# Kernel optimization log

Hardware: AMD Instinct MI355X
Metric: run time of the kernel (lower is better)

The kernel has to match this reference:

```python
import jax, jax.numpy as jnp
import numpy as np

N = 100000      # nodes
E = 1600000     # graph edges
P = 800000      # hypergraph incidence pairs
HE = 20000      # hyperedges
F_IN = 128      # node features
DIM = 64        # hidden dim (hard-coded in module)
NC = 40         # num_classes


def _lin_init(key, fan_in, fan_out):
    k1, k2 = jax.random.split(key)
    s = 1.0 / np.sqrt(fan_in)
    W = jax.random.uniform(k1, (fan_in, fan_out), jnp.float32, -s, s)
    b = jax.random.uniform(k2, (fan_out,), jnp.float32, -s, s)
    return W, b


def setup_inputs() -> dict:
    key = jax.random.key(0)
    ks = jax.random.split(key, 10)
    x = jax.random.normal(ks[0], (N, F_IN), jnp.float32)
    edge_index = jax.random.randint(ks[1], (2, E), 0, N, dtype=jnp.int64)
    node_idx = jax.random.randint(ks[2], (P,), 0, N, dtype=jnp.int64)
    he_idx = jax.random.randint(ks[3], (P,), 0, HE, dtype=jnp.int64)
    hyperedge_index = jnp.stack([node_idx, he_idx], axis=0)
    W_h1, b_h1 = _lin_init(ks[4], F_IN, DIM)
    W_h2, b_h2 = _lin_init(ks[5], DIM, DIM)
    W_c1, b_c1 = _lin_init(ks[6], F_IN + DIM, DIM)
    W_c2, b_c2 = _lin_init(ks[7], DIM, NC)
    W_lp, b_lp = _lin_init(ks[8], NC, NC)
    return dict(x=x, edge_index=edge_index, hyperedge_index=hyperedge_index,
                W_h1=W_h1, b_h1=b_h1, W_h2=W_h2, b_h2=b_h2,
                W_c1=W_c1, b_c1=b_c1, W_c2=W_c2, b_c2=b_c2,
                W_lp=W_lp, b_lp=b_lp)


def hypergraph_conv(x, node_idx, he_idx, W, b):
    # PyG HypergraphConv (no attention, hyperedge_weight = 1):
    # out = D^{-1} H B^{-1} H^T (x W) + b
    xw = x @ W                                    # [N, D]
    ones = jnp.ones(node_idx.shape[0], xw.dtype)
    Dn = jax.ops.segment_sum(ones, node_idx, num_segments=N)   # node degree
    Bh = jax.ops.segment_sum(ones, he_idx, num_segments=HE)    # hyperedge size
    D_inv = jnp.where(Dn > 0, 1.0 / Dn, 0.0)
    B_inv = jnp.where(Bh > 0, 1.0 / Bh, 0.0)
    # node -> hyperedge: m_e = (1/|e|) sum_{i in e} xw[i]
    msg1 = xw[node_idx] * B_inv[he_idx][:, None]               # [P, D]
    e_feat = jax.ops.segment_sum(msg1, he_idx, num_segments=HE)
    # hyperedge -> node: out_i = (1/deg(i)) sum_{e ni i} m_e
    msg2 = e_feat[he_idx] * D_inv[node_idx][:, None]           # [P, D]
    out = jax.ops.segment_sum(msg2, node_idx, num_segments=N)
    return out + b


def gcn_conv(x, edge_index, W, b):
    # PyG GCNConv: add self-loops, symmetric normalization
    xw = x @ W                                    # [N, D]
    loop = jnp.arange(N, dtype=edge_index.dtype)
    src = jnp.concatenate([edge_index[0], loop])
    dst = jnp.concatenate([edge_index[1], loop])
    deg = jax.ops.segment_sum(jnp.ones(dst.shape[0], xw.dtype), dst, num_segments=N)
    dis = jnp.where(deg > 0, jax.lax.rsqrt(deg), 0.0)
    norm = dis[src] * dis[dst]                    # [E+N]
    out = jax.ops.segment_sum(xw[src] * norm[:, None], dst, num_segments=N)
    return out + b


def reference(x, edge_index, hyperedge_index,
              W_h1, b_h1, W_h2, b_h2, W_c1, b_c1, W_c2, b_c2, W_lp, b_lp):
    node_idx, he_idx = hyperedge_index[0], hyperedge_index[1]
    x_hyper = jax.nn.relu(hypergraph_conv(x, node_idx, he_idx, W_h1, b_h1))
    # dropout is identity in eval mode
    x_hyper = hypergraph_conv(x_hyper, node_idx, he_idx, W_h2, b_h2)
    xc = jnp.concatenate([x, x_hyper], axis=1)    # [N, F_IN + DIM]
    x_gnn = jax.nn.relu(gcn_conv(xc, edge_index, W_c1, b_c1))
    x_gnn = gcn_conv(x_gnn, edge_index, W_c2, b_c2)
    return x_gnn @ W_lp + b_lp                     # [N, NC]
```

## Files before the change

### kernel.cpp

```cpp
#include <hip/hip_runtime.h>
#include <hip/hip_bf16.h>


typedef __attribute__((ext_vector_type(8))) short s16x8;
typedef __attribute__((ext_vector_type(4))) float f32x4;

__device__ __forceinline__ float ldf(const void* p, int f32, long long i) {
    if (f32) return ((const float*)p)[i];
    unsigned v = ((unsigned)((const unsigned short*)p)[i]) << 16;
    return __uint_as_float(v);
}

__device__ __forceinline__ int ldi(const int* __restrict__ w, int i64, long long i, int lim) {
    int v = i64 ? w[2 * i] : w[i];
    return ((unsigned)v < (unsigned)lim) ? v : 0;
}

__device__ __forceinline__ float b2f(unsigned short u) {
    return __uint_as_float(((unsigned)u) << 16);
}
__device__ __forceinline__ unsigned short f2b(float f) {
    __hip_bfloat16 h = __float2bfloat16(f);
    return *reinterpret_cast<unsigned short*>(&h);
}
__device__ __forceinline__ float4 b2f4(ushort4 u) {
    return make_float4(b2f(u.x), b2f(u.y), b2f(u.z), b2f(u.w));
}
__device__ __forceinline__ ushort4 f2b4(float4 v) {
    ushort4 u; u.x = f2b(v.x); u.y = f2b(v.y); u.z = f2b(v.z); u.w = f2b(v.w);
    return u;
}

struct DPtrs { const void* p[13]; int n[13]; };

__global__ void detect_k(DPtrs dp, int* __restrict__ flags) {
    int b = blockIdx.x;
    __shared__ int cnt;
    if (threadIdx.x == 0) cnt = 0;
    __syncthreads();
    int c = 0;
    if (b < 11) {
        const unsigned short* u = (const unsigned short*)dp.p[b];
        int np = dp.n[b]; if (np > 2048) np = 2048;
        for (int i = threadIdx.x; i < np; i += blockDim.x) {
            unsigned e = (u[i] >> 7) & 0xFFu;
            if (e != 0u && (e < 90u || e > 160u)) c++;
        }
        atomicAdd(&cnt, c);
        __syncthreads();
        if (threadIdx.x == 0) flags[b] = (cnt * 8 > np) ? 1 : 0;
    } else {
        const int* w = (const int*)dp.p[b];
        int np = dp.n[b]; if (np > 1024) np = 1024;
        for (int i = threadIdx.x; i < np; i += blockDim.x)
            if (w[2 * i + 1] != 0) c++;
        atomicAdd(&cnt, c);
        __syncthreads();
        if (threadIdx.x == 0) flags[b] = (cnt == 0) ? 1 : 0;
    }
}

struct Item { int b1; unsigned p1; int b2; unsigned p2; };

__device__ __forceinline__ Item decode(const int* __restrict__ ew, const int* __restrict__ hw,
                                       const int* __restrict__ FL, long long i,
                                       int E, int P, int N, int HE, int shN, int shH) {
    Item it; it.b2 = -1; it.p2 = 0;
    if (i < E) {
        int g = FL[11];
        int key = ldi(ew, g, (long long)E + i, N);
        int val = ldi(ew, g, i, N);
        it.b1 = key >> shN;
        it.p1 = ((unsigned)(key & ((1 << shN) - 1)) << 20) | (unsigned)val;
    } else {
        long long j = i - E;
        int g = FL[12];
        int nd = ldi(hw, g, j, N);
        int he = ldi(hw, g, (long long)P + j, HE);
        it.b1 = 256 + (nd >> shN);
        it.p1 = ((unsigned)(nd & ((1 << shN) - 1)) << 20) | (unsigned)he;
        it.b2 = 512 + (he >> shH);
        it.p2 = ((unsigned)(he & ((1 << shH) - 1)) << 20) | (unsigned)nd;
    }
    return it;
}

__global__ void bucket_count_k(const int* __restrict__ ew, const int* __restrict__ hw,
                               const int* __restrict__ FL, int* __restrict__ gcnt,
                               int E, int P, int N, int HE, int shN, int shH) {
    __shared__ int hist[768];
    int t = threadIdx.x;
    for (int b = t; b < 768; b += 256) hist[b] = 0;
    __syncthreads();
    long long T = (long long)E + P;
    long long stride = (long long)gridDim.x * 256;
    for (long long i = (long long)blockIdx.x * 256 + t; i < T; i += stride) {
        Item it = decode(ew, hw, FL, i, E, P, N, HE, shN, shH);
        atomicAdd(&hist[it.b1], 1);
        if (it.b2 >= 0) atomicAdd(&hist[it.b2], 1);
    }
    __syncthreads();
    for (int b = t; b < 768; b += 256) {
        int h = hist[b];
        if (h) atomicAdd(&gcnt[b], h);
    }
}

__global__ void bucket_scan_k(const int* __restrict__ gcnt, int* __restrict__ bkOff,
                              int* __restrict__ gcur, int E, int P) {
    __shared__ int sh[256];
    int t = threadIdx.x;
    long long rbase[3] = {0, (long long)E, (long long)E + P};
    for (int c = 0; c < 3; c++) {
        int v = gcnt[c * 256 + t];
        sh[t] = v;
        __syncthreads();
        for (int o = 1; o < 256; o <<= 1) {
            int y = (t >= o) ? sh[t - o] : 0;
            __syncthreads();
            sh[t] += y;
            __syncthreads();
        }
        int excl = sh[t] - v;
        bkOff[c * 256 + t] = excl;
        gcur[c * 256 + t] = (int)(rbase[c] + excl);
        __syncthreads();
    }
}

#define PCHUNK 8192

__global__ void bucket_place_k(const int* __restrict__ ew, const int* __restrict__ hw,
                               const int* __restrict__ FL, int* __restrict__ gcur,
                               unsigned* __restrict__ pbuf,
                               int E, int P, int N, int HE, int shN, int shH) {
    __shared__ int hist[768];
    __shared__ int cur[768];
    long long T = (long long)E + P;
    long long start = (long long)blockIdx.x * PCHUNK;
    long long end = start + PCHUNK; if (end > T) end = T;
    int t = threadIdx.x;
    for (int b = t; b < 768; b += 256) hist[b] = 0;
    __syncthreads();
    for (long long i = start + t; i < end; i += 256) {
        Item it = decode(ew, hw, FL, i, E, P, N, HE, shN, shH);
        atomicAdd(&hist[it.b1], 1);
        if (it.b2 >= 0) atomicAdd(&hist[it.b2], 1);
    }
    __syncthreads();
    for (int b = t; b < 768; b += 256) {
        int h = hist[b];
        cur[b] = h ? atomicAdd(&gcur[b], h) : 0;
    }
    __syncthreads();
    for (long long i = start + t; i < end; i += 256) {
        Item it = decode(ew, hw, FL, i, E, P, N, HE, shN, shH);
        int s1 = atomicAdd(&cur[it.b1], 1);
        pbuf[s1] = it.p1;
        if (it.b2 >= 0) {
            int s2 = atomicAdd(&cur[it.b2], 1);
            pbuf[s2] = it.p2;
        }
    }
}

__global__ void build_k(const unsigned* __restrict__ pbuf,
                        const int* __restrict__ gcnt, const int* __restrict__ bkOff,
                        int* __restrict__ eoff, int* __restrict__ ecnt, int* __restrict__ esrc,
                        int* __restrict__ poffN, int* __restrict__ pcntN, int* __restrict__ pheL,
                        int* __restrict__ poffH, int* __restrict__ pcntH, int* __restrict__ pniL,
                        int E, int P, int N, int HE, int shN, int shH) {
    __shared__ int hist[512];
    __shared__ int offs[512];
    __shared__ int s2[256];
    int b = blockIdx.x, t = threadIdx.x;
    int csr = b >> 8, lb = b & 255;
    int sh    = (csr == 2) ? shH : shN;
    int nkeys = (csr == 2) ? HE : N;
    int span = 1 << sh;
    int keyBase = lb << sh;
    if (keyBase >= nkeys) return;
    int keyEnd = keyBase + span; if (keyEnd > nkeys) keyEnd = nkeys;
    int cnt = gcnt[b];
    long long rbase = (csr == 0) ? 0 : ((csr == 1) ? (long long)E : (long long)E + P);
    long long pstart = rbase + bkOff[b];
    int lstBase = bkOff[b];
    int* off  = (csr == 0) ? eoff : ((csr == 1) ? poffN : poffH);
    int* cntA = (csr == 0) ? ecnt : ((csr == 1) ? pcntN : pcntH);
    int* lst  = (csr == 0) ? esrc : ((csr == 1) ? pheL : pniL);

    for (int k = t; k < 512; k += 256) hist[k] = 0;
    __syncthreads();
    for (int i = t; i < cnt; i += 256)
        atomicAdd(&hist[pbuf[pstart + i] >> 20], 1);
    __syncthreads();
    int a0 = hist[2 * t], a1 = hist[2 * t + 1];
    s2[t] = a0 + a1;
    __syncthreads();
    for (int o = 1; o < 256; o <<= 1) {
        int y = (t >= o) ? s2[t - o] : 0;
        __syncthreads();
        s2[t] += y;
        __syncthreads();
    }
    int excl = s2[t] - (a0 + a1);
    offs[2 * t] = excl;
    offs[2 * t + 1] = excl + a0;
    __syncthreads();
    for (int k = keyBase + t; k < keyEnd; k += 256) {
        off[k]  = lstBase + offs[k - keyBase];
        cntA[k] = hist[k - keyBase];
    }
    __syncthreads();
    for (int i = t; i < cnt; i += 256) {
        unsigned u = pbuf[pstart + i];
        int lk = u >> 20;
        int slot = atomicAdd(&offs[lk], 1);
        lst[lstBase + slot] = (int)(u & 0xFFFFFu);
    }
}

__global__ void norms_k(const int* __restrict__ ecnt, const int* __restrict__ pcntN,
                        const int* __restrict__ pcntH, float* __restrict__ dis,
                        float* __restrict__ Dinv, float* __restrict__ Binv, int N, int HE) {
    int i = blockIdx.x * blockDim.x + threadIdx.x;
    if (i < N) dis[i] = rsqrtf((float)(ecnt[i] + 1));
    else if (i < 2 * N) { int c = pcntN[i - N]; Dinv[i - N] = c ? (1.f / (float)c) : 0.f; }
    else if (i < 2 * N + HE) { int c = pcntH[i - 2 * N]; Binv[i - 2 * N] = c ? (1.f / (float)c) : 0.f; }
}

__global__ void wlp2_k(const void* Wc2, const int* fWc2, const void* Wlp, const int* fWlp,
                       const void* bc2, const int* fbc2, const void* blp, const int* fblp,
                       float* __restrict__ Wlp2, float* __restrict__ bias2, int NC) {
    extern __shared__ float sm[];
    float* sW2 = sm;
    float* sLP = sm + 64 * NC;
    int t = threadIdx.x;
    int fw2 = fWc2[0], flp = fWlp[0];
    for (int e = t; e < 64 * NC; e += blockDim.x) sW2[e] = ldf(Wc2, fw2, e);
    for (int e = t; e < NC * NC; e += blockDim.x) sLP[e] = ldf(Wlp, flp, e);
    __syncthreads();
    for (int e = t; e < 64 * NC; e += blockDim.x) {
        int r = e / NC, c = e % NC;
        float s = 0.f;
        for (int k = 0; k < NC; k++) s = fmaf(sW2[r * NC + k], sLP[k * NC + c], s);
        Wlp2[e] = s;
    }
    if (t < NC) {
        float s = ldf(blp, fblp[0], t);
        int fb2 = fbc2[0];
        for (int k = 0; k < NC; k++) s = fmaf(ldf(bc2, fb2, k), sLP[k * NC + t], s);
        bias2[t] = s;
    }
}

__global__ void gat_n2e_k(const ushort4* __restrict__ xw, const int* __restrict__ off,
                          const int* __restrict__ cnt, const int* __restrict__ lst,
                          const float* __restrict__ Binv, ushort4* __restrict__ ef, int HE) {
    int idx = blockIdx.x * blockDim.x + threadIdx.x;
    int e = idx >> 4, l = idx & 15;
    if (e >= HE) return;
    int o = off[e], c = cnt[e];
    float4 a = make_float4(0.f, 0.f, 0.f, 0.f);
    int j = 0;
    for (; j + 4 <= c; j += 4) {
        int s0 = lst[o + j], s1 = lst[o + j + 1], s2 = lst[o + j + 2], s3 = lst[o + j + 3];
        float4 v0 = b2f4(xw[((long long)s0 << 4) + l]);
        float4 v1 = b2f4(xw[((long long)s1 << 4) + l]);
        float4 v2 = b2f4(xw[((long long)s2 << 4) + l]);
        float4 v3 = b2f4(xw[((long long)s3 << 4) + l]);
        a.x += (v0.x + v1.x) + (v2.x + v3.x);
        a.y += (v0.y + v1.y) + (v2.y + v3.y);
        a.z += (v0.z + v1.z) + (v2.z + v3.z);
        a.w += (v0.w + v1.w) + (v2.w + v3.w);
    }
    for (; j < c; j++) {
        float4 v = b2f4(xw[((long long)lst[o + j] << 4) + l]);
        a.x += v.x; a.y += v.y; a.z += v.z; a.w += v.w;
    }
    float bi = Binv[e];
    a.x *= bi; a.y *= bi; a.z *= bi; a.w *= bi;
    ef[((long long)e << 4) + l] = f2b4(a);
}

template <bool RELU>
__global__ void gat_e2n_k(const ushort4* __restrict__ ef, const int* __restrict__ off,
                          const int* __restrict__ cnt, const int* __restrict__ lst,
                          const float* __restrict__ Dinv, const void* __restrict__ bias,
                          const int* __restrict__ fb, ushort4* __restrict__ out, int N) {
    int idx = blockIdx.x * blockDim.x + threadIdx.x;
    int w = idx >> 4, l = idx & 15;
    if (w >= N) return;
    int o = off[w], c = cnt[w];
    float4 a = make_float4(0.f, 0.f, 0.f, 0.f);
    int j = 0;
    for (; j + 4 <= c; j += 4) {
        int s0 = lst[o + j], s1 = lst[o + j + 1], s2 = lst[o + j + 2], s3 = lst[o + j + 3];
        float4 v0 = b2f4(ef[((long long)s0 << 4) + l]);
        float4 v1 = b2f4(ef[((long long)s1 << 4) + l]);
        float4 v2 = b2f4(ef[((long long)s2 << 4) + l]);
        float4 v3 = b2f4(ef[((long long)s3 << 4) + l]);
        a.x += (v0.x + v1.x) + (v2.x + v3.x);
        a.y += (v0.y + v1.y) + (v2.y + v3.y);
        a.z += (v0.z + v1.z) + (v2.z + v3.z);
        a.w += (v0.w + v1.w) + (v2.w + v3.w);
    }
    for (; j < c; j++) {
        float4 v = b2f4(ef[((long long)lst[o + j] << 4) + l]);
        a.x += v.x; a.y += v.y; a.z += v.z; a.w += v.w;
    }
    float di = Dinv[w];
    int fbv = fb[0];
    float4 b = make_float4(ldf(bias, fbv, 4 * l), ldf(bias, fbv, 4 * l + 1),
                           ldf(bias, fbv, 4 * l + 2), ldf(bias, fbv, 4 * l + 3));
    a.x = a.x * di + b.x; a.y = a.y * di + b.y;
    a.z = a.z * di + b.z; a.w = a.w * di + b.w;
    if (RELU) {
        a.x = fmaxf(a.x, 0.f); a.y = fmaxf(a.y, 0.f);
        a.z = fmaxf(a.z, 0.f); a.w = fmaxf(a.w, 0.f);
    }
    out[((long long)w << 4) + l] = f2b4(a);
}

template <bool RELU>
__global__ void gcn_gat_k(const ushort4* __restrict__ y, const int* __restrict__ off,
                          const int* __restrict__ cnt, const int* __restrict__ lst,
                          const float* __restrict__ dis, const void* __restrict__ bias,
                          const int* __restrict__ fb, ushort4* __restrict__ out, int N) {
    int idx = blockIdx.x * blockDim.x + threadIdx.x;
    int w = idx >> 4, l = idx & 15;
    if (w >= N) return;
    int o = off[w], c = cnt[w];
    float4 a = b2f4(y[((long long)w << 4) + l]);
    int j = 0;
    for (; j + 4 <= c; j += 4) {
        int s0 = lst[o + j], s1 = lst[o + j + 1], s2 = lst[o + j + 2], s3 = lst[o + j + 3];
        float4 v0 = b2f4(y[((long long)s0 << 4) + l]);
        float4 v1 = b2f4(y[((long long)s1 << 4) + l]);
        float4 v2 = b2f4(y[((long long)s2 << 4) + l]);
        float4 v3 = b2f4(y[((long long)s3 << 4) + l]);
        a.x += (v0.x + v1.x) + (v2.x + v3.x);
        a.y += (v0.y + v1.y) + (v2.y + v3.y);
        a.z += (v0.z + v1.z) + (v2.z + v3.z);
        a.w += (v0.w + v1.w) + (v2.w + v3.w);
    }
    for (; j < c; j++) {
        float4 v = b2f4(y[((long long)lst[o + j] << 4) + l]);
        a.x += v.x; a.y += v.y; a.z += v.z; a.w += v.w;
    }
    float dd = dis[w];
    int fbv = fb[0];
    float4 b = make_float4(ldf(bias, fbv, 4 * l), ldf(bias, fbv, 4 * l + 1),
                           ldf(bias, fbv, 4 * l + 2), ldf(bias, fbv, 4 * l + 3));
    a.x = a.x * dd + b.x; a.y = a.y * dd + b.y;
    a.z = a.z * dd + b.z; a.w = a.w * dd + b.w;
    if (RELU) {
        a.x = fmaxf(a.x, 0.f); a.y = fmaxf(a.y, 0.f);
        a.z = fmaxf(a.z, 0.f); a.w = fmaxf(a.w, 0.f);
    }
    out[((long long)w << 4) + l] = f2b4(a);
}

__global__ void gcn_gatM_k(const ushort4* __restrict__ y2, const int* __restrict__ off,
                           const int* __restrict__ cnt, const int* __restrict__ lst,
                           const float* __restrict__ dis, const float* __restrict__ bias2,
                           float4* __restrict__ out4, int N, int nc4, int npw) {
    int idx = blockIdx.x * blockDim.x + threadIdx.x;
    int wave = idx >> 6, l64 = idx & 63;
    int grp = l64 / 10, li = l64 - grp * 10;
    if (nc4 != 10) { grp = l64 / nc4; li = l64 - grp * nc4; }
    int w = wave * npw + grp;
    if (grp >= npw || w >= N) return;
    int o = off[w], c = cnt[w];
    float4 a = b2f4(y2[(long long)w * nc4 + li]);
    int j = 0;
    for (; j + 4 <= c; j += 4) {
        int s0 = lst[o + j], s1 = lst[o + j + 1], s2 = lst[o + j + 2], s3 = lst[o + j + 3];
        float4 v0 = b2f4(y2[(long long)s0 * nc4 + li]);
        float4 v1 = b2f4(y2[(long long)s1 * nc4 + li]);
        float4 v2 = b2f4(y2[(long long)s2 * nc4 + li]);
        float4 v3 = b2f4(y2[(long long)s3 * nc4 + li]);
        a.x += (v0.x + v1.x) + (v2.x + v3.x);
        a.y += (v0.y + v1.y) + (v2.y + v3.y);
        a.z += (v0.z + v1.z) + (v2.z + v3.z);
        a.w += (v0.w + v1.w) + (v2.w + v3.w);
    }
    for (; j < c; j++) {
        float4 v = b2f4(y2[(long long)lst[o + j] * nc4 + li]);
        a.x += v.x; a.y += v.y; a.z += v.z; a.w += v.w;
    }
    float dd = dis[w];
    float4 b = *(const float4*)&bias2[4 * li];
    a.x = a.x * dd + b.x; a.y = a.y * dd + b.y;
    a.z = a.z * dd + b.z; a.w = a.w * dd + b.w;
    out4[(long long)w * nc4 + li] = a;
}

__device__ __forceinline__ s16x8 load8bf(const void* A, int af, long long base) {
    s16x8 o;
    if (af) {
        float4 v0 = *(const float4*)((const float*)A + base);
        float4 v1 = *(const float4*)((const float*)A + base + 4);
        o[0] = (short)f2b(v0.x); o[1] = (short)f2b(v0.y);
        o[2] = (short)f2b(v0.z); o[3] = (short)f2b(v0.w);
        o[4] = (short)f2b(v1.x); o[5] = (short)f2b(v1.y);
        o[6] = (short)f2b(v1.z); o[7] = (short)f2b(v1.w);
    } else {
        o = *(const s16x8*)&((const unsigned short*)A)[base];
    }
    return o;
}

template <int KK, int MM, bool CATMODE, bool ABF16, bool SCALE>
__global__ __launch_bounds__(256)
void gemm_mfma_k(const void* __restrict__ A, const int* __restrict__ fA,
                 const unsigned short* __restrict__ A2,
                 const void* __restrict__ B, const int* __restrict__ fB,
                 const float* __restrict__ dscale,
                 unsigned short* __restrict__ C, int NR) {
    constexpr int BM = 128;
    constexpr int Kp = KK + 8;
    constexpr int MT = (MM + 15) / 16;
    constexpr int CPR = KK / 8;
    static_assert(KK % 32 == 0, "K must be multiple of 32");

    __shared__ __align__(16) unsigned short As[BM * Kp];
    __shared__ __align__(16) unsigned short Bs[MT * 16 * Kp];

    const int t = threadIdx.x;
    const long long m0 = (long long)blockIdx.x * BM;
    const int af = fA ? fA[0] : 1;
    const int bfv = fB ? fB[0] : 1;

    for (int idx = t; idx < BM * CPR; idx += 256) {
        int r = idx / CPR;
        int kc = (idx - r * CPR) * 8;
        long long gr = m0 + r;
        s16x8 v = {0, 0, 0, 0, 0, 0, 0, 0};
        if (gr < NR) {
            if constexpr (CATMODE) {
                if (kc < 128) v = load8bf(A, af, gr * 128 + kc);
                else v = *(const s16x8*)&A2[gr * 64 + (kc - 128)];
            } else if constexpr (ABF16) {
                v = *(const s16x8*)&((const unsigned short*)A)[gr * KK + kc];
            } else {
                v = load8bf(A, af, gr * (long long)KK + kc);
            }
        }
        *(s16x8*)&As[r * Kp + kc] = v;
    }

    for (int e = t; e < KK * MM; e += 256) {
        int k = e / MM;
        int n = e - k * MM;
        Bs[n * Kp + k] = f2b(ldf(B, bfv, e));
    }
    if constexpr (MT * 16 != MM) {
        for (int e = t; e < (MT * 16 - MM) * KK; e += 256) {
            int n = MM + e / KK;
            int k = e - (e / KK) * KK;
            Bs[n * Kp + k] = 0;
        }
    }
    __syncthreads();

    const int wid = t >> 6, lane = t & 63;
    const int r0 = wid * 32;
    const int arow = lane & 15;
    const int kgrp = lane >> 4;

    f32x4 acc0[MT] = {};
    f32x4 acc1[MT] = {};
#pragma unroll
    for (int kc = 0; kc < KK; kc += 32) {
        const int kb = kc + kgrp * 8;
        s16x8 a0 = *(const s16x8*)&As[(r0 + arow) * Kp + kb];
        s16x8 a1 = *(const s16x8*)&As[(r0 + 16 + arow) * Kp + kb];
#pragma unroll
        for (int m = 0; m < MT; m++) {
            s16x8 b = *(const s16x8*)&Bs[(m * 16 + arow) * Kp + kb];
            acc0[m] = __builtin_amdgcn_mfma_f32_16x16x32_bf16(a0, b, acc0[m], 0, 0, 0);
            acc1[m] = __builtin_amdgcn_mfma_f32_16x16x32_bf16(a1, b, acc1[m], 0, 0, 0);
        }
    }

    const int col0 = lane & 15;
    const int rsub = (lane >> 4) * 4;
#pragma unroll
    for (int h = 0; h < 2; h++) {
#pragma unroll
        for (int i = 0; i < 4; i++) {
            long long r = m0 + r0 + h * 16 + rsub + i;
            if (r < NR) {
                float s = SCALE ? dscale[r] : 1.f;
#pragma unroll
                for (int m = 0; m < MT; m++) {
                    int col = m * 16 + col0;
                    float val = h ? acc1[m][i] : acc0[m][i];
                    if (MT * 16 == MM || col < MM)
                        C[r * MM + col] = f2b(val * s);
                }
            }
        }
    }
}

static inline dim3 g1d(long long n, int b) { return dim3((unsigned)((n + b - 1) / b)); }
static inline int imin(int a, int b) { return a < b ? a : b; }

extern "C" void kernel_launch(void* const* d_in, const int* in_sizes, int n_in,
                              void* d_out, int out_size, void* d_ws, size_t ws_size,
                              hipStream_t stream) {
    const int N  = in_sizes[0] / 128;
    const int E  = in_sizes[1] / 2;
    const int P  = in_sizes[2] / 2;
    const int HE = 20000;
    const int NC = in_sizes[9] / 64;
    const int nc4 = NC / 4;
    const int npw = 64 / nc4;

    const void* x    = d_in[0];
    const int*  ew   = (const int*)d_in[1];
    const int*  hw   = (const int*)d_in[2];
    const void* W_h1 = d_in[3];
    const void* b_h1 = d_in[4];
    const void* W_h2 = d_in[5];
    const void* b_h2 = d_in[6];
    const void* W_c1 = d_in[7];
    const void* b_c1 = d_in[8];
    const void* W_c2 = d_in[9];
    const void* b_c2 = d_in[10];
    const void* W_lp = d_in[11];
    const void* b_lp = d_in[12];

    int shN = 0; while (((N - 1) >> shN) >= 256) shN++;
    int shH = 0; while (((HE - 1) >> shH) >= 256) shH++;

    char* wp = (char*)d_ws;
    auto allocF = [&](size_t n) { float* p = (float*)wp; wp += n * 4; return p; };
    auto allocI = [&](size_t n) { int* p = (int*)wp; wp += n * 4; return p; };
    unsigned short* ub  = (unsigned short*)allocF((size_t)N * 32);
    unsigned short* hb  = (unsigned short*)allocF((size_t)N * 32);
    unsigned short* efb = (unsigned short*)allocF((size_t)HE * 32);
    float* dis   = allocF(N);
    float* Dinv  = allocF(N);
    float* Binv  = allocF(HE);
    float* Wlp2  = allocF((size_t)64 * NC);
    float* bias2 = allocF(NC);
    int* ecnt  = allocI(N);
    int* pcntN = allocI(N);
    int* pcntH = allocI(HE);
    int* eoff  = allocI(N);
    int* poffN = allocI(N);
    int* poffH = allocI(HE);
    int* esrc  = allocI(E);
    int* pheL  = allocI(P);
    int* pniL  = allocI(P);
    int* gBkt  = allocI(768);
    int* bkOff = allocI(768);
    int* gcur  = allocI(768);
    int* FL    = allocI(16);
    unsigned* pbuf = (unsigned*)allocI((size_t)E + 2 * (size_t)P);

    dim3 b256(256), d1(1);

    DPtrs dp;
    const void* farr[11] = {x, W_h1, b_h1, W_h2, b_h2, W_c1, b_c1, W_c2, b_c2, W_lp, b_lp};
    const int   fsz[11]  = {in_sizes[0], in_sizes[3], in_sizes[4], in_sizes[5], in_sizes[6],
                            in_sizes[7], in_sizes[8], in_sizes[9], in_sizes[10], in_sizes[11],
                            in_sizes[12]};
    for (int i = 0; i < 11; ++i) { dp.p[i] = farr[i]; dp.n[i] = fsz[i]; }
    dp.p[11] = ew; dp.n[11] = imin(E, 1024);
    dp.p[12] = hw; dp.n[12] = imin(P, 1024);
    detect_k<<<dim3(13), b256, 0, stream>>>(dp, FL);
    const int* fX   = FL + 0;
    const int* fWh1 = FL + 1,  *fbh1 = FL + 2;
    const int* fWh2 = FL + 3,  *fbh2 = FL + 4;
    const int* fWc1 = FL + 5,  *fbc1 = FL + 6;
    const int* fWc2 = FL + 7,  *fbc2 = FL + 8;
    const int* fWlp = FL + 9,  *fblp = FL + 10;

    hipMemsetAsync(gBkt, 0, 768 * 4, stream);
    bucket_count_k<<<dim3(512), b256, 0, stream>>>(ew, hw, FL, gBkt, E, P, N, HE, shN, shH);
    bucket_scan_k<<<d1, b256, 0, stream>>>(gBkt, bkOff, gcur, E, P);
    {
        long long T = (long long)E + P;
        int nChunks = (int)((T + PCHUNK - 1) / PCHUNK);
        bucket_place_k<<<dim3(nChunks), b256, 0, stream>>>(ew, hw, FL, gcur, pbuf,
                                                           E, P, N, HE, shN, shH);
    }
    build_k<<<dim3(768), b256, 0, stream>>>(pbuf, gBkt, bkOff,
                                            eoff, ecnt, esrc,
                                            poffN, pcntN, pheL,
                                            poffH, pcntH, pniL,
                                            E, P, N, HE, shN, shH);

    norms_k<<<g1d(2 * N + HE, 256), b256, 0, stream>>>(ecnt, pcntN, pcntH, dis, Dinv, Binv, N, HE);
    wlp2_k<<<d1, b256, (64 * NC + NC * NC) * 4, stream>>>(
        W_c2, fWc2, W_lp, fWlp, b_c2, fbc2, b_lp, fblp, Wlp2, bias2, NC);

    const dim3 mfmaGrid((N + 127) / 128);
    const dim3 gatN16(g1d((long long)N * 16, 256));
    const dim3 gatH16(g1d((long long)HE * 16, 256));
    const dim3 gatNC(g1d((long long)((N + npw - 1) / npw) * 64, 256));

    gemm_mfma_k<128, 64, false, false, false><<<mfmaGrid, b256, 0, stream>>>(
        x, fX, nullptr, W_h1, fWh1, nullptr, ub, N);
    gat_n2e_k<<<gatH16, b256, 0, stream>>>((const ushort4*)ub, poffH, pcntH, pniL, Binv, (ushort4*)efb, HE);
    gat_e2n_k<true><<<gatN16, b256, 0, stream>>>((const ushort4*)efb, poffN, pcntN, pheL, Dinv, b_h1, fbh1, (ushort4*)hb, N);

    gemm_mfma_k<64, 64, false, true, false><<<mfmaGrid, b256, 0, stream>>>(
        hb, nullptr, nullptr, W_h2, fWh2, nullptr, ub, N);
    gat_n2e_k<<<gatH16, b256, 0, stream>>>((const ushort4*)ub, poffH, pcntH, pniL, Binv, (ushort4*)efb, HE);
    gat_e2n_k<false><<<gatN16, b256, 0, stream>>>((const ushort4*)efb, poffN, pcntN, pheL, Dinv, b_h2, fbh2, (ushort4*)hb, N);

    gemm_mfma_k<192, 64, true, false, true><<<mfmaGrid, b256, 0, stream>>>(
        x, fX, hb, W_c1, fWc1, dis, ub, N);
    gcn_gat_k<true><<<gatN16, b256, 0, stream>>>((const ushort4*)ub, eoff, ecnt, esrc, dis, b_c1, fbc1, (ushort4*)hb, N);

    gemm_mfma_k<64, 40, false, true, true><<<mfmaGrid, b256, 0, stream>>>(
        hb, nullptr, nullptr, Wlp2, nullptr, dis, ub, N);
    gcn_gatM_k<<<gatNC, b256, 0, stream>>>((const ushort4*)ub, eoff, ecnt, esrc, dis, bias2, (float4*)d_out, N, nc4, npw);
}
```

Baseline: 485.4 us.

## Pretranspose weights once and load GEMM operands directly from global memory

Adds a small kernel that converts and transposes all four weight matrices to padded bf16 once, so each GEMM block no longer transposes the weights into LDS. The GEMM now reads A fragments and the pretransposed B directly from global memory per wave, with no shared memory or block barrier. Out-of-range rows are clamped instead of zero-filled. Also shrinks the bucket placement chunk size to launch more blocks. The risk is that uncoalesced global fragment loads and repeated B reads through cache replace the previously staged LDS tiles.

New measurement: 472.9 us. -2.6%, faster.

```diff
diff --git a/kernel.cpp b/kernel.cpp
--- a/kernel.cpp
+++ b/kernel.cpp
@@ -128,7 +128,7 @@
     }
 }
 
-#define PCHUNK 8192
+#define PCHUNK 2048
 
 __global__ void bucket_place_k(const int* __restrict__ ew, const int* __restrict__ hw,
                                const int* __restrict__ FL, int* __restrict__ gcur,
@@ -254,6 +254,19 @@
     }
 }
 
+struct BP { const void* B; const int* fB; int K; int M; int Mp; unsigned short* out; };
+
+__global__ void bprep_k(BP p0, BP p1, BP p2, BP p3) {
+    BP p = (blockIdx.x == 0) ? p0 : (blockIdx.x == 1) ? p1 : (blockIdx.x == 2) ? p2 : p3;
+    int fb = p.fB ? p.fB[0] : 1;
+    int tot = p.Mp * p.K;
+    for (int e = threadIdx.x; e < tot; e += blockDim.x) {
+        int m = e / p.K, k = e - m * p.K;
+        float v = (m < p.M) ? ldf(p.B, fb, (long long)k * p.M + m) : 0.f;
+        p.out[e] = f2b(v);
+    }
+}
+
 __global__ void gat_n2e_k(const ushort4* __restrict__ xw, const int* __restrict__ off,
                           const int* __restrict__ cnt, const int* __restrict__ lst,
                           const float* __restrict__ Binv, ushort4* __restrict__ ef, int HE) {
@@ -413,72 +426,49 @@
 
 template <int KK, int MM, bool CATMODE, bool ABF16, bool SCALE>
 __global__ __launch_bounds__(256)
-void gemm_mfma_k(const void* __restrict__ A, const int* __restrict__ fA,
-                 const unsigned short* __restrict__ A2,
-                 const void* __restrict__ B, const int* __restrict__ fB,
-                 const float* __restrict__ dscale,
-                 unsigned short* __restrict__ C, int NR) {
-    constexpr int BM = 128;
-    constexpr int Kp = KK + 8;
+void gemm_mfma2_k(const void* __restrict__ A, const int* __restrict__ fA,
+                  const unsigned short* __restrict__ A2,
+                  const unsigned short* __restrict__ Bt,
+                  const float* __restrict__ dscale,
+                  unsigned short* __restrict__ C, int NR) {
     constexpr int MT = (MM + 15) / 16;
-    constexpr int CPR = KK / 8;
     static_assert(KK % 32 == 0, "K must be multiple of 32");
 
-    __shared__ __align__(16) unsigned short As[BM * Kp];
-    __shared__ __align__(16) unsigned short Bs[MT * 16 * Kp];
-
     const int t = threadIdx.x;
-    const long long m0 = (long long)blockIdx.x * BM;
+    const int wid = t >> 6, lane = t & 63;
+    const long long r0 = ((long long)blockIdx.x * 4 + wid) * 32;
+    if (r0 >= NR) return;
+
     const int af = fA ? fA[0] : 1;
-    const int bfv = fB ? fB[0] : 1;
-
-    for (int idx = t; idx < BM * CPR; idx += 256) {
-        int r = idx / CPR;
-        int kc = (idx - r * CPR) * 8;
-        long long gr = m0 + r;
-        s16x8 v = {0, 0, 0, 0, 0, 0, 0, 0};
-        if (gr < NR) {
-            if constexpr (CATMODE) {
-                if (kc < 128) v = load8bf(A, af, gr * 128 + kc);
-                else v = *(const s16x8*)&A2[gr * 64 + (kc - 128)];
-            } else if constexpr (ABF16) {
-                v = *(const s16x8*)&((const unsigned short*)A)[gr * KK + kc];
-            } else {
-                v = load8bf(A, af, gr * (long long)KK + kc);
-            }
-        }
-        *(s16x8*)&As[r * Kp + kc] = v;
-    }
-
-    for (int e = t; e < KK * MM; e += 256) {
-        int k = e / MM;
-        int n = e - k * MM;
-        Bs[n * Kp + k] = f2b(ldf(B, bfv, e));
-    }
-    if constexpr (MT * 16 != MM) {
-        for (int e = t; e < (MT * 16 - MM) * KK; e += 256) {
-            int n = MM + e / KK;
-            int k = e - (e / KK) * KK;
-            Bs[n * Kp + k] = 0;
-        }
-    }
-    __syncthreads();
-
-    const int wid = t >> 6, lane = t & 63;
-    const int r0 = wid * 32;
     const int arow = lane & 15;
     const int kgrp = lane >> 4;
+    long long ra = r0 + arow;      if (ra > NR - 1) ra = NR - 1;
+    long long rb = r0 + 16 + arow; if (rb > NR - 1) rb = NR - 1;
 
     f32x4 acc0[MT] = {};
     f32x4 acc1[MT] = {};
 #pragma unroll
     for (int kc = 0; kc < KK; kc += 32) {
         const int kb = kc + kgrp * 8;
-        s16x8 a0 = *(const s16x8*)&As[(r0 + arow) * Kp + kb];
-        s16x8 a1 = *(const s16x8*)&As[(r0 + 16 + arow) * Kp + kb];
+        s16x8 a0, a1;
+        if constexpr (CATMODE) {
+            if (kc < 128) {
+                a0 = load8bf(A, af, ra * 128 + kb);
+                a1 = load8bf(A, af, rb * 128 + kb);
+            } else {
+                a0 = *(const s16x8*)&A2[ra * 64 + (kb - 128)];
+                a1 = *(const s16x8*)&A2[rb * 64 + (kb - 128)];
+            }
+        } else if constexpr (ABF16) {
+            a0 = *(const s16x8*)&((const unsigned short*)A)[ra * KK + kb];
+            a1 = *(const s16x8*)&((const unsigned short*)A)[rb * KK + kb];
+        } else {
+            a0 = load8bf(A, af, ra * (long long)KK + kb);
+            a1 = load8bf(A, af, rb * (long long)KK + kb);
+        }
 #pragma unroll
         for (int m = 0; m < MT; m++) {
-            s16x8 b = *(const s16x8*)&Bs[(m * 16 + arow) * Kp + kb];
+            s16x8 b = *(const s16x8*)&Bt[(m * 16 + arow) * KK + kb];
             acc0[m] = __builtin_amdgcn_mfma_f32_16x16x32_bf16(a0, b, acc0[m], 0, 0, 0);
             acc1[m] = __builtin_amdgcn_mfma_f32_16x16x32_bf16(a1, b, acc1[m], 0, 0, 0);
         }
@@ -490,7 +480,7 @@
     for (int h = 0; h < 2; h++) {
 #pragma unroll
         for (int i = 0; i < 4; i++) {
-            long long r = m0 + r0 + h * 16 + rsub + i;
+            long long r = r0 + h * 16 + rsub + i;
             if (r < NR) {
                 float s = SCALE ? dscale[r] : 1.f;
 #pragma unroll
@@ -547,6 +537,10 @@
     float* Binv  = allocF(HE);
     float* Wlp2  = allocF((size_t)64 * NC);
     float* bias2 = allocF(NC);
+    unsigned short* bt1 = (unsigned short*)allocF((size_t)64 * 128 / 2);
+    unsigned short* bt2 = (unsigned short*)allocF((size_t)64 * 64 / 2);
+    unsigned short* btc = (unsigned short*)allocF((size_t)64 * 192 / 2);
+    unsigned short* btl = (unsigned short*)allocF((size_t)48 * 64 / 2);
     int* ecnt  = allocI(N);
     int* pcntN = allocI(N);
     int* pcntH = allocI(HE);
@@ -598,27 +592,34 @@
     norms_k<<<g1d(2 * N + HE, 256), b256, 0, stream>>>(ecnt, pcntN, pcntH, dis, Dinv, Binv, N, HE);
     wlp2_k<<<d1, b256, (64 * NC + NC * NC) * 4, stream>>>(
         W_c2, fWc2, W_lp, fWlp, b_c2, fbc2, b_lp, fblp, Wlp2, bias2, NC);
+    {
+        BP p0 = {W_h1, fWh1, 128, 64, 64, bt1};
+        BP p1 = {W_h2, fWh2,  64, 64, 64, bt2};
+        BP p2 = {W_c1, fWc1, 192, 64, 64, btc};
+        BP p3 = {Wlp2, nullptr, 64, NC, 48, btl};
+        bprep_k<<<dim3(4), b256, 0, stream>>>(p0, p1, p2, p3);
+    }
 
     const dim3 mfmaGrid((N + 127) / 128);
     const dim3 gatN16(g1d((long long)N * 16, 256));
     const dim3 gatH16(g1d((long long)HE * 16, 256));
     const dim3 gatNC(g1d((long long)((N + npw - 1) / npw) * 64, 256));
 
-    gemm_mfma_k<128, 64, false, false, false><<<mfmaGrid, b256, 0, stream>>>(
-        x, fX, nullptr, W_h1, fWh1, nullptr, ub, N);
+    gemm_mfma2_k<128, 64, false, false, false><<<mfmaGrid, b256, 0, stream>>>(
+        x, fX, nullptr, bt1, nullptr, ub, N);
     gat_n2e_k<<<gatH16, b256, 0, stream>>>((const ushort4*)ub, poffH, pcntH, pniL, Binv, (ushort4*)efb, HE);
     gat_e2n_k<true><<<gatN16, b256, 0, stream>>>((const ushort4*)efb, poffN, pcntN, pheL, Dinv, b_h1, fbh1, (ushort4*)hb, N);
 
-    gemm_mfma_k<64, 64, false, true, false><<<mfmaGrid, b256, 0, stream>>>(
-        hb, nullptr, nullptr, W_h2, fWh2, nullptr, ub, N);
+    gemm_mfma2_k<64, 64, false, true, false><<<mfmaGrid, b256, 0, stream>>>(
+        hb, nullptr, nullptr, bt2, nullptr, ub, N);
     gat_n2e_k<<<gatH16, b256, 0, stream>>>((const ushort4*)ub, poffH, pcntH, pniL, Binv, (ushort4*)efb, HE);
     gat_e2n_k<false><<<gatN16, b256, 0, stream>>>((const ushort4*)efb, poffN, pcntN, pheL, Dinv, b_h2, fbh2, (ushort4*)hb, N);
 
-    gemm_mfma_k<192, 64, true, false, true><<<mfmaGrid, b256, 0, stream>>>(
-        x, fX, hb, W_c1, fWc1, dis, ub, N);
+    gemm_mfma2_k<192, 64, true, false, true><<<mfmaGrid, b256, 0, stream>>>(
+        x, fX, hb, btc, dis, ub, N);
     gcn_gat_k<true><<<gatN16, b256, 0, stream>>>((const ushort4*)ub, eoff, ecnt, esrc, dis, b_c1, fbc1, (ushort4*)hb, N);
 
-    gemm_mfma_k<64, 40, false, true, true><<<mfmaGrid, b256, 0, stream>>>(
-        hb, nullptr, nullptr, Wlp2, nullptr, dis, ub, N);
+    gemm_mfma2_k<64, 40, false, true, true><<<mfmaGrid, b256, 0, stream>>>(
+        hb, nullptr, nullptr, btl, dis, ub, N);
     gcn_gatM_k<<<gatNC, b256, 0, stream>>>((const ushort4*)ub, eoff, ecnt, esrc, dis, bias2, (float4*)d_out, N, nc4, npw);
 }
```
